# Kernel tuning notes

Measured on AMD Instinct MI355X. Metric: run time of the kernel, lower is better.

The kernel has to match this reference:

```python
import jax, jax.numpy as jnp
import numpy as np

LAMBDA_COOR = 5.0
LAMBDA_NOOBJ = 0.5


def setup_inputs() -> dict:
    key = jax.random.key(0)
    k1, k2 = jax.random.split(key)
    B, W, H, C = 128, 256, 256, 5
    outputs = jax.random.normal(k1, (B, W, H, C), dtype=jnp.float32)
    targets = jax.random.normal(k2, (B, W, H, C), dtype=jnp.float32)
    return {"outputs": outputs, "targets": targets}


def reference(outputs, targets):
    # channel layout per cell: (conf, x, y, w, h)
    conf_pred = outputs[..., 0]
    conf_gt = targets[..., 0]
    obj_mask = conf_gt > 0
    # sum of squared coord errors (x, y, w, h) per cell: [B, W, H]
    coord_sq = jnp.sum((outputs[..., 1:] - targets[..., 1:]) ** 2, axis=-1)
    obj_loss = LAMBDA_COOR * coord_sq + (conf_pred - 1.0) ** 2
    noobj_loss = LAMBDA_NOOBJ * conf_pred ** 2
    loss = jnp.sum(jnp.where(obj_mask, obj_loss, noobj_loss))
    return loss / outputs.shape[0]
```

## Files before the change

kernel.cpp:

```cpp
#include <hip/hip_runtime.h>

#define LAMBDA_COOR 5.0f
#define LAMBDA_NOOBJ 0.5f

constexpr int TPB = 256;

typedef float v4f __attribute__((ext_vector_type(4)));

__global__ __launch_bounds__(TPB) void yolo_loss_kernel(
    const v4f* __restrict__ o4, const v4f* __restrict__ t4,
    float* __restrict__ loss, float inv_b)
{
    const size_t g = (size_t)blockIdx.x * TPB + threadIdx.x;
    const v4f* ob = o4 + g * 5;
    const v4f* tb = t4 + g * 5;

    v4f vo[5], vt[5];
    #pragma unroll
    for (int k = 0; k < 5; ++k) {
        vo[k] = ob[k];
        vt[k] = tb[k];
    }

    float o[20], t[20];
    #pragma unroll
    for (int k = 0; k < 5; ++k) {
        #pragma unroll
        for (int j = 0; j < 4; ++j) {
            o[4 * k + j] = vo[k][j];
            t[4 * k + j] = vt[k][j];
        }
    }

    float acc = 0.0f;
    #pragma unroll
    for (int c = 0; c < 4; ++c) {
        const float* oc = o + 5 * c;
        const float* tc = t + 5 * c;
        float conf = oc[0];
        float coord = 0.0f;
        #pragma unroll
        for (int k = 1; k < 5; ++k) {
            float d = oc[k] - tc[k];
            coord = fmaf(d, d, coord);
        }
        float obj   = fmaf(LAMBDA_COOR, coord, (conf - 1.0f) * (conf - 1.0f));
        float noobj = LAMBDA_NOOBJ * conf * conf;
        acc += (tc[0] > 0.0f) ? obj : noobj;
    }

    #pragma unroll
    for (int off = 32; off > 0; off >>= 1)
        acc += __shfl_down(acc, off, 64);

    __shared__ float wave_sums[TPB / 64];
    const int lane = threadIdx.x & 63;
    const int wid  = threadIdx.x >> 6;
    if (lane == 0) wave_sums[wid] = acc;
    __syncthreads();

    if (threadIdx.x == 0) {
        float s = 0.0f;
        #pragma unroll
        for (int i = 0; i < TPB / 64; ++i) s += wave_sums[i];
        atomicAdd(loss, s * inv_b);
    }
}

extern "C" void kernel_launch(void* const* d_in, const int* in_sizes, int n_in,
                              void* d_out, int out_size, void* d_ws, size_t ws_size,
                              hipStream_t stream) {
    const v4f* outputs = (const v4f*)d_in[0];
    const v4f* targets = (const v4f*)d_in[1];
    float* loss = (float*)d_out;

    const int n_elems  = in_sizes[0];
    const int n_groups = n_elems / 20;
    const int blocks   = n_groups / TPB;
    const float inv_b  = 1.0f / 128.0f;

    hipMemsetAsync(d_out, 0, sizeof(float), stream);

    yolo_loss_kernel<<<blocks, TPB, 0, stream>>>(outputs, targets, loss, inv_b);
}
```

Measured before the change: 346.8 us.

## Stage input tiles through LDS with direct global-to-LDS loads for coalescing

Result: no change. 344.4 us (-0.7%).

```diff
diff --git a/kernel.cpp b/kernel.cpp
--- a/kernel.cpp
+++ b/kernel.cpp
@@ -4,39 +4,57 @@
 #define LAMBDA_NOOBJ 0.5f
 
 constexpr int TPB = 256;
+constexpr int WPB = TPB / 64;
+constexpr int TILE_F = 1280;
 
 typedef float v4f __attribute__((ext_vector_type(4)));
 
 __global__ __launch_bounds__(TPB) void yolo_loss_kernel(
-    const v4f* __restrict__ o4, const v4f* __restrict__ t4,
+    const float* __restrict__ o, const float* __restrict__ t,
     float* __restrict__ loss, float inv_b)
 {
-    const size_t g = (size_t)blockIdx.x * TPB + threadIdx.x;
-    const v4f* ob = o4 + g * 5;
-    const v4f* tb = t4 + g * 5;
+    __shared__ __align__(16) float so[WPB][TILE_F];
+    __shared__ __align__(16) float st[WPB][TILE_F];
 
-    v4f vo[5], vt[5];
+    const int lane = threadIdx.x & 63;
+    const int wid  = threadIdx.x >> 6;
+    const size_t wtile = (size_t)blockIdx.x * WPB + wid;
+
+    const float* ob = o + wtile * TILE_F + lane * 4;
+    const float* tb = t + wtile * TILE_F + lane * 4;
+
     #pragma unroll
     for (int k = 0; k < 5; ++k) {
-        vo[k] = ob[k];
-        vt[k] = tb[k];
+        __builtin_amdgcn_global_load_lds(
+            (__attribute__((address_space(1))) void*)(ob + k * 256),
+            (__attribute__((address_space(3))) void*)&so[wid][k * 256],
+            16, 0, 0);
+        __builtin_amdgcn_global_load_lds(
+            (__attribute__((address_space(1))) void*)(tb + k * 256),
+            (__attribute__((address_space(3))) void*)&st[wid][k * 256],
+            16, 0, 0);
     }
+    __builtin_amdgcn_s_waitcnt(0);
 
-    float o[20], t[20];
+    const v4f* lo4 = (const v4f*)&so[wid][20 * lane];
+    const v4f* lt4 = (const v4f*)&st[wid][20 * lane];
+    float ov[20], tv[20];
     #pragma unroll
     for (int k = 0; k < 5; ++k) {
+        v4f a = lo4[k];
+        v4f b = lt4[k];
         #pragma unroll
         for (int j = 0; j < 4; ++j) {
-            o[4 * k + j] = vo[k][j];
-            t[4 * k + j] = vt[k][j];
+            ov[4 * k + j] = a[j];
+            tv[4 * k + j] = b[j];
         }
     }
 
     float acc = 0.0f;
     #pragma unroll
     for (int c = 0; c < 4; ++c) {
-        const float* oc = o + 5 * c;
-        const float* tc = t + 5 * c;
+        const float* oc = ov + 5 * c;
+        const float* tc = tv + 5 * c;
         float conf = oc[0];
         float coord = 0.0f;
         #pragma unroll
@@ -53,16 +71,14 @@
     for (int off = 32; off > 0; off >>= 1)
         acc += __shfl_down(acc, off, 64);
 
-    __shared__ float wave_sums[TPB / 64];
-    const int lane = threadIdx.x & 63;
-    const int wid  = threadIdx.x >> 6;
+    __shared__ float wave_sums[WPB];
     if (lane == 0) wave_sums[wid] = acc;
     __syncthreads();
 
     if (threadIdx.x == 0) {
         float s = 0.0f;
         #pragma unroll
-        for (int i = 0; i < TPB / 64; ++i) s += wave_sums[i];
+        for (int i = 0; i < WPB; ++i) s += wave_sums[i];
         atomicAdd(loss, s * inv_b);
     }
 }
@@ -70,13 +86,13 @@
 extern "C" void kernel_launch(void* const* d_in, const int* in_sizes, int n_in,
                               void* d_out, int out_size, void* d_ws, size_t ws_size,
                               hipStream_t stream) {
-    const v4f* outputs = (const v4f*)d_in[0];
-    const v4f* targets = (const v4f*)d_in[1];
+    const float* outputs = (const float*)d_in[0];
+    const float* targets = (const float*)d_in[1];
     float* loss = (float*)d_out;
 
     const int n_elems  = in_sizes[0];
-    const int n_groups = n_elems / 20;
-    const int blocks   = n_groups / TPB;
+    const int n_wtiles = n_elems / TILE_F;
+    const int blocks   = n_wtiles / WPB;
     const float inv_b  = 1.0f / 128.0f;
 
     hipMemsetAsync(d_out, 0, sizeof(float), stream);
```
